# Kernel optimization log

Hardware: AMD Instinct MI355X
Metric: run time of the kernel (lower is better)

Reference implementation:

```python
import jax, jax.numpy as jnp
import numpy as np

B, H, KV, HD, D, S = 8, 32, 8, 128, 4096, 4096
PAST = S - 2  # 4094, cache nearly full
ROPE_THETA = 10000.0


def rotate_half(x):
    h = x.shape[-1] // 2
    return jnp.concatenate([-x[..., h:], x[..., :h]], axis=-1)


def setup_inputs() -> dict:
    key = jax.random.key(0)
    ks = jax.random.split(key, 10)
    hidden_states = jax.random.normal(ks[0], (B, 1, D), jnp.float32)
    # HF additive causal mask for decode: 0 where position is valid, -inf-ish beyond
    pos = jnp.arange(S)
    attention_mask = jnp.broadcast_to(
        jnp.where(pos < PAST + 1, 0.0, -1e9).astype(jnp.float32)[None, None, None, :],
        (B, 1, 1, S),
    )
    # RoPE cos/sin for the single decoded position (position id = PAST)
    inv_freq = 1.0 / (ROPE_THETA ** (jnp.arange(0, HD, 2, dtype=jnp.float32) / HD))
    ang = PAST * inv_freq  # [HD/2]
    emb = jnp.concatenate([ang, ang], axis=-1)  # [HD]
    cos = jnp.broadcast_to(jnp.cos(emb)[None, None, :], (B, 1, HD)).astype(jnp.float32)
    sin = jnp.broadcast_to(jnp.sin(emb)[None, None, :], (B, 1, HD)).astype(jnp.float32)
    past_key = jax.random.normal(ks[1], (B, KV, PAST, HD), jnp.float32)
    past_value = jax.random.normal(ks[2], (B, KV, PAST, HD), jnp.float32)
    k_cache = jax.random.normal(ks[3], (B, KV, S, HD), jnp.float32)
    v_cache = jax.random.normal(ks[4], (B, KV, S, HD), jnp.float32)
    Wq = jax.random.normal(ks[5], (D, H * HD), jnp.float32) * 0.02
    Wk = jax.random.normal(ks[6], (D, KV * HD), jnp.float32) * 0.02
    Wv = jax.random.normal(ks[7], (D, KV * HD), jnp.float32) * 0.02
    Wo = jax.random.normal(ks[8], (H * HD, D), jnp.float32) * 0.02
    return dict(hidden_states=hidden_states, attention_mask=attention_mask, cos=cos,
                sin=sin, past_key=past_key, past_value=past_value,
                k_cache=k_cache, v_cache=v_cache, Wq=Wq, Wk=Wk, Wv=Wv, Wo=Wo)


def reference(hidden_states, attention_mask, cos, sin, past_key, past_value,
              k_cache, v_cache, Wq, Wk, Wv, Wo):
    b = hidden_states.shape[0]
    past_len = past_key.shape[2]  # static
    # q/k/v projections for the single decode token
    q = (hidden_states @ Wq).reshape(b, 1, H, HD).transpose(0, 2, 1, 3)   # [B,H,1,hd]
    k = (hidden_states @ Wk).reshape(b, 1, KV, HD).transpose(0, 2, 1, 3)  # [B,KV,1,hd]
    v = (hidden_states @ Wv).reshape(b, 1, KV, HD).transpose(0, 2, 1, 3)
    # rotary: cos/sin [B,1,hd] -> unsqueeze head dim -> [B,1,1,hd]
    c = cos[:, None, :, :]
    s = sin[:, None, :, :]
    q = q * c + rotate_half(q) * s
    k = k * c + rotate_half(k) * s
    # StaticCache: scatter past K/V into positions [0, past_len), new token at past_len
    kf = k_cache.at[:, :, :past_len, :].set(past_key)
    kf = kf.at[:, :, past_len:past_len + 1, :].set(k)
    vf = v_cache.at[:, :, :past_len, :].set(past_value)
    vf = vf.at[:, :, past_len:past_len + 1, :].set(v)
    # GQA: repeat kv heads
    n_rep = H // KV
    kr = jnp.repeat(kf, n_rep, axis=1)  # [B,H,S,hd]
    vr = jnp.repeat(vf, n_rep, axis=1)
    scores = jnp.einsum('bhqd,bhkd->bhqk', q, kr) / np.float32(np.sqrt(HD))
    scores = scores + attention_mask  # [B,1,1,S] broadcasts over heads
    probs = jax.nn.softmax(scores.astype(jnp.float32), axis=-1).astype(q.dtype)
    out = jnp.einsum('bhqk,bhkd->bhqd', probs, vr)  # [B,H,1,hd]
    out = out.transpose(0, 2, 1, 3).reshape(b, 1, H * HD)
    return out @ Wo  # [B,1,D]
```

## Files before the change

### kernel.cpp

```cpp
#include <hip/hip_runtime.h>

#define BB 8
#define HH 32
#define KVH 8
#define HD 128
#define DD 4096
#define PAST 4094
#define QCOLS 4096
#define KVCOLS 1024
#define NC_QKV 6144
#define DCH 64
#define NDCH 64
#define CHUNK 32
#define NCHUNK 128
#define QSCALE 0.08838834764831845f
#define FIN_PER_B 3584

__global__ __launch_bounds__(256)
void matvec_partial(const float* __restrict__ hin,
                    const float* __restrict__ W0,
                    const float* __restrict__ W1,
                    const float* __restrict__ W2,
                    int c_w1, int c_w2, int NC,
                    float* __restrict__ part)
{
    __shared__ float hl[DCH][BB];
    const int tid = threadIdx.x;
    const int d0 = blockIdx.y * DCH;
    const int cb = blockIdx.x * 512;

    for (int idx = tid; idx < DCH * BB; idx += 256) {
        int dd = idx & (DCH - 1);
        int b = idx >> 6;
        hl[dd][b] = hin[b * DD + d0 + dd];
    }
    __syncthreads();

    const int c = cb + tid * 2;
    const float* W;
    int ldw, cl;
    if (c < c_w1)      { W = W0; ldw = c_w1;        cl = c; }
    else if (c < c_w2) { W = W1; ldw = c_w2 - c_w1; cl = c - c_w1; }
    else               { W = W2; ldw = NC - c_w2;   cl = c - c_w2; }
    const float* wp = W + (size_t)d0 * ldw + cl;

    float2 acc[BB];
    #pragma unroll
    for (int b = 0; b < BB; ++b) { acc[b].x = 0.f; acc[b].y = 0.f; }

    #pragma unroll 8
    for (int dd = 0; dd < DCH; ++dd) {
        float2 w = *(const float2*)wp;
        wp += ldw;
        float hv[8];
        *(float4*)&hv[0] = *(const float4*)&hl[dd][0];
        *(float4*)&hv[4] = *(const float4*)&hl[dd][4];
        #pragma unroll
        for (int b = 0; b < BB; ++b) {
            acc[b].x = fmaf(hv[b], w.x, acc[b].x);
            acc[b].y = fmaf(hv[b], w.y, acc[b].y);
        }
    }

    float* po = part + (size_t)blockIdx.y * (BB * NC) + c;
    #pragma unroll
    for (int b = 0; b < BB; ++b) {
        *(float2*)(po + (size_t)b * NC) = acc[b];
    }
}

__global__ __launch_bounds__(256)
void qkv_finish(const float* __restrict__ part,
                const float* __restrict__ cosv,
                const float* __restrict__ sinv,
                float* __restrict__ qout,
                float* __restrict__ knew,
                float* __restrict__ vnew)
{
    __shared__ float red[4][64][2];
    const int lane = threadIdx.x & 63;
    const int w = threadIdx.x >> 6;
    const int o = blockIdx.x * 64 + lane;
    const int b = o / FIN_PER_B;
    const int r = o - b * FIN_PER_B;

    float s0 = 0.f, s1 = 0.f;
    if (r < 2560) {
        const int hd = r & 63;
        const int head = r >> 6;
        const int c_lo = head * HD + hd;
        const float* p0 = part + (size_t)b * NC_QKV + c_lo;
        const float* p1 = p0 + 64;
        #pragma unroll 16
        for (int i = w * 16; i < w * 16 + 16; ++i) {
            s0 += p0[(size_t)i * (BB * NC_QKV)];
            s1 += p1[(size_t)i * (BB * NC_QKV)];
        }
    } else {
        const int c = r - 2560 + QCOLS + KVCOLS;
        const float* p = part + (size_t)b * NC_QKV + c;
        #pragma unroll 16
        for (int i = w * 16; i < w * 16 + 16; ++i)
            s0 += p[(size_t)i * (BB * NC_QKV)];
    }
    red[w][lane][0] = s0;
    red[w][lane][1] = s1;
    __syncthreads();

    if (threadIdx.x < 64) {
        const float a0 = red[0][lane][0] + red[1][lane][0]
                       + red[2][lane][0] + red[3][lane][0];
        const float a1 = red[0][lane][1] + red[1][lane][1]
                       + red[2][lane][1] + red[3][lane][1];
        if (r < 2560) {
            const int hd = r & 63;
            const int head = r >> 6;
            const int c_lo = head * HD + hd;
            const float cs_lo = cosv[b * HD + hd];
            const float sn_lo = sinv[b * HD + hd];
            const float cs_hi = cosv[b * HD + hd + 64];
            const float sn_hi = sinv[b * HD + hd + 64];
            const float v_lo = fmaf(a0, cs_lo, -a1 * sn_lo);
            const float v_hi = fmaf(a1, cs_hi,  a0 * sn_hi);
            if (c_lo < QCOLS) {
                qout[b * QCOLS + c_lo]      = v_lo * QSCALE;
                qout[b * QCOLS + c_lo + 64] = v_hi * QSCALE;
            } else {
                knew[b * KVCOLS + (c_lo - QCOLS)]      = v_lo;
                knew[b * KVCOLS + (c_lo - QCOLS) + 64] = v_hi;
            }
        } else {
            const int c = r - 2560;
            vnew[b * KVCOLS + c] = a0;
        }
    }
}

__global__ __launch_bounds__(256, 8)
void attn_partial(const float* __restrict__ past_key,
                  const float* __restrict__ past_value,
                  const float* __restrict__ q,
                  const float* __restrict__ knew,
                  const float* __restrict__ vnew,
                  float* __restrict__ pacc,
                  float* __restrict__ pl)
{
    const int pair = blockIdx.x;
    const int wid = threadIdx.x >> 6;
    const int chunk = blockIdx.y * 4 + wid;
    const int b = pair >> 3;
    const int kv = pair & 7;
    const int lane = threadIdx.x & 63;
    const int half = lane >> 5;
    const int lh = lane & 31;

    const float* qb = q + b * QCOLS + (kv * 4) * HD + 4 * lh;
    const float4 qv0 = *(const float4*)(qb);
    const float4 qv1 = *(const float4*)(qb + HD);
    const float4 qv2 = *(const float4*)(qb + 2 * HD);
    const float4 qv3 = *(const float4*)(qb + 3 * HD);

    const float* kb = past_key   + (size_t)pair * PAST * HD;
    const float* vb = past_value + (size_t)pair * PAST * HD;

    float4 acc0 = {0,0,0,0}, acc1 = {0,0,0,0}, acc2 = {0,0,0,0}, acc3 = {0,0,0,0};
    float l0 = 0.f, l1 = 0.f, l2 = 0.f, l3 = 0.f;

    const int jbase = chunk * CHUNK + half;

    if (chunk < NCHUNK - 1) {
        const float* kp = kb + (size_t)jbase * HD + 4 * lh;
        const float* vp = vb + (size_t)jbase * HD + 4 * lh;
        #pragma unroll 4
        for (int it = 0; it < 16; ++it) {
            const float4 kk = *(const float4*)kp;  kp += 2 * HD;
            float s0 = kk.x*qv0.x + kk.y*qv0.y + kk.z*qv0.z + kk.w*qv0.w;
            float s1 = kk.x*qv1.x + kk.y*qv1.y + kk.z*qv1.z + kk.w*qv1.w;
            float s2 = kk.x*qv2.x + kk.y*qv2.y + kk.z*qv2.z + kk.w*qv2.w;
            float s3 = kk.x*qv3.x + kk.y*qv3.y + kk.z*qv3.z + kk.w*qv3.w;
            #pragma unroll
            for (int m = 1; m <= 16; m <<= 1) {
                s0 += __shfl_xor(s0, m, 64);
                s1 += __shfl_xor(s1, m, 64);
                s2 += __shfl_xor(s2, m, 64);
                s3 += __shfl_xor(s3, m, 64);
            }
            const float4 vv = *(const float4*)vp;  vp += 2 * HD;
            const float p0 = __expf(s0);
            const float p1 = __expf(s1);
            const float p2 = __expf(s2);
            const float p3 = __expf(s3);
            l0 += p0; l1 += p1; l2 += p2; l3 += p3;
            acc0.x = fmaf(p0, vv.x, acc0.x); acc0.y = fmaf(p0, vv.y, acc0.y);
            acc0.z = fmaf(p0, vv.z, acc0.z); acc0.w = fmaf(p0, vv.w, acc0.w);
            acc1.x = fmaf(p1, vv.x, acc1.x); acc1.y = fmaf(p1, vv.y, acc1.y);
            acc1.z = fmaf(p1, vv.z, acc1.z); acc1.w = fmaf(p1, vv.w, acc1.w);
            acc2.x = fmaf(p2, vv.x, acc2.x); acc2.y = fmaf(p2, vv.y, acc2.y);
            acc2.z = fmaf(p2, vv.z, acc2.z); acc2.w = fmaf(p2, vv.w, acc2.w);
            acc3.x = fmaf(p3, vv.x, acc3.x); acc3.y = fmaf(p3, vv.y, acc3.y);
            acc3.z = fmaf(p3, vv.z, acc3.z); acc3.w = fmaf(p3, vv.w, acc3.w);
        }
    } else {
        const float* kn = knew + pair * HD;
        const float* vn = vnew + pair * HD;
        #pragma unroll 2
        for (int it = 0; it < 16; ++it) {
            const int j = jbase + it * 2;
            const bool valid = (j <= PAST);
            const float* kp;
            const float* vp;
            if (j < PAST) { kp = kb + (size_t)j * HD; vp = vb + (size_t)j * HD; }
            else          { kp = kn;                   vp = vn; }

            const float4 kk = *(const float4*)(kp + 4 * lh);
            float s0 = kk.x*qv0.x + kk.y*qv0.y + kk.z*qv0.z + kk.w*qv0.w;
            float s1 = kk.x*qv1.x + kk.y*qv1.y + kk.z*qv1.z + kk.w*qv1.w;
            float s2 = kk.x*qv2.x + kk.y*qv2.y + kk.z*qv2.z + kk.w*qv2.w;
            float s3 = kk.x*qv3.x + kk.y*qv3.y + kk.z*qv3.z + kk.w*qv3.w;
            #pragma unroll
            for (int m = 1; m <= 16; m <<= 1) {
                s0 += __shfl_xor(s0, m, 64);
                s1 += __shfl_xor(s1, m, 64);
                s2 += __shfl_xor(s2, m, 64);
                s3 += __shfl_xor(s3, m, 64);
            }
            const float4 vv = *(const float4*)(vp + 4 * lh);
            const float p0 = valid ? __expf(s0) : 0.f;
            const float p1 = valid ? __expf(s1) : 0.f;
            const float p2 = valid ? __expf(s2) : 0.f;
            const float p3 = valid ? __expf(s3) : 0.f;
            l0 += p0; l1 += p1; l2 += p2; l3 += p3;
            acc0.x = fmaf(p0, vv.x, acc0.x); acc0.y = fmaf(p0, vv.y, acc0.y);
            acc0.z = fmaf(p0, vv.z, acc0.z); acc0.w = fmaf(p0, vv.w, acc0.w);
            acc1.x = fmaf(p1, vv.x, acc1.x); acc1.y = fmaf(p1, vv.y, acc1.y);
            acc1.z = fmaf(p1, vv.z, acc1.z); acc1.w = fmaf(p1, vv.w, acc1.w);
            acc2.x = fmaf(p2, vv.x, acc2.x); acc2.y = fmaf(p2, vv.y, acc2.y);
            acc2.z = fmaf(p2, vv.z, acc2.z); acc2.w = fmaf(p2, vv.w, acc2.w);
            acc3.x = fmaf(p3, vv.x, acc3.x); acc3.y = fmaf(p3, vv.y, acc3.y);
            acc3.z = fmaf(p3, vv.z, acc3.z); acc3.w = fmaf(p3, vv.w, acc3.w);
        }
    }

    l0 += __shfl_xor(l0, 32, 64);
    l1 += __shfl_xor(l1, 32, 64);
    l2 += __shfl_xor(l2, 32, 64);
    l3 += __shfl_xor(l3, 32, 64);
    acc0.x += __shfl_xor(acc0.x, 32, 64); acc0.y += __shfl_xor(acc0.y, 32, 64);
    acc0.z += __shfl_xor(acc0.z, 32, 64); acc0.w += __shfl_xor(acc0.w, 32, 64);
    acc1.x += __shfl_xor(acc1.x, 32, 64); acc1.y += __shfl_xor(acc1.y, 32, 64);
    acc1.z += __shfl_xor(acc1.z, 32, 64); acc1.w += __shfl_xor(acc1.w, 32, 64);
    acc2.x += __shfl_xor(acc2.x, 32, 64); acc2.y += __shfl_xor(acc2.y, 32, 64);
    acc2.z += __shfl_xor(acc2.z, 32, 64); acc2.w += __shfl_xor(acc2.w, 32, 64);
    acc3.x += __shfl_xor(acc3.x, 32, 64); acc3.y += __shfl_xor(acc3.y, 32, 64);
    acc3.z += __shfl_xor(acc3.z, 32, 64); acc3.w += __shfl_xor(acc3.w, 32, 64);

    if (half == 0) {
        float* po = pacc + (((size_t)pair * NCHUNK + chunk) * 4) * HD + 4 * lh;
        *(float4*)(po)          = acc0;
        *(float4*)(po + HD)     = acc1;
        *(float4*)(po + 2*HD)   = acc2;
        *(float4*)(po + 3*HD)   = acc3;
        if (lh == 0) {
            float* plo = pl + ((size_t)pair * NCHUNK + chunk) * 4;
            plo[0] = l0; plo[1] = l1; plo[2] = l2; plo[3] = l3;
        }
    }
}

__global__ __launch_bounds__(256)
void attn_combine(const float* __restrict__ pacc,
                  const float* __restrict__ pl,
                  float* __restrict__ attn_out)
{
    __shared__ float racc[4][64];
    __shared__ float rl[4];
    const int lane = threadIdx.x & 63;
    const int w = threadIdx.x >> 6;
    const int o = blockIdx.x * 64 + lane;
    const int d = o & 127;
    const int h = (o >> 7) & 31;
    const int b = o >> 12;
    const int kv = h >> 2;
    const int qi = h & 3;
    const int pair = b * 8 + kv;

    const float* pa  = pacc + ((size_t)pair * NCHUNK * 4 + qi) * HD + d;
    const float* pls = pl + (size_t)pair * NCHUNK * 4 + qi;
    float acc = 0.f, lsum = 0.f;
    #pragma unroll 8
    for (int c = w * 32; c < w * 32 + 32; ++c) {
        acc  += pa[(size_t)c * 4 * HD];
        lsum += pls[c * 4];
    }
    racc[w][lane] = acc;
    if (lane == 0) rl[w] = lsum;
    __syncthreads();
    if (threadIdx.x < 64) {
        const float a = racc[0][lane] + racc[1][lane]
                      + racc[2][lane] + racc[3][lane];
        const float L = rl[0] + rl[1] + rl[2] + rl[3];
        attn_out[b * QCOLS + h * HD + d] = a / L;
    }
}

__global__ __launch_bounds__(256)
void wo_finish(const float* __restrict__ part, float* __restrict__ out)
{
    __shared__ float red[4][64];
    const int lane = threadIdx.x & 63;
    const int w = threadIdx.x >> 6;
    const int o = blockIdx.x * 64 + lane;
    const float* p = part + o;
    float s = 0.f;
    #pragma unroll 16
    for (int i = w * 16; i < w * 16 + 16; ++i)
        s += p[(size_t)i * (BB * QCOLS)];
    red[w][lane] = s;
    __syncthreads();
    if (threadIdx.x < 64) {
        out[o] = red[0][lane] + red[1][lane] + red[2][lane] + red[3][lane];
    }
}

extern "C" void kernel_launch(void* const* d_in, const int* in_sizes, int n_in,
                              void* d_out, int out_size, void* d_ws, size_t ws_size,
                              hipStream_t stream)
{
    (void)in_sizes; (void)n_in; (void)out_size; (void)ws_size;
    const float* hidden     = (const float*)d_in[0];
    const float* cosv       = (const float*)d_in[2];
    const float* sinv       = (const float*)d_in[3];
    const float* past_key   = (const float*)d_in[4];
    const float* past_value = (const float*)d_in[5];
    const float* Wq = (const float*)d_in[8];
    const float* Wk = (const float*)d_in[9];
    const float* Wv = (const float*)d_in[10];
    const float* Wo = (const float*)d_in[11];
    float* out = (float*)d_out;
    float* ws  = (float*)d_ws;

    float* qkv_part = ws;
    float* qrope    = qkv_part + (size_t)NDCH * BB * NC_QKV;
    float* knew     = qrope + BB * QCOLS;
    float* vnew     = knew + BB * KVCOLS;
    float* pacc     = vnew + BB * KVCOLS;
    float* pl       = pacc + (size_t)64 * NCHUNK * 4 * HD;
    float* attn_out = pl + (size_t)64 * NCHUNK * 4;
    float* wo_part  = qkv_part;

    matvec_partial<<<dim3(12, NDCH), 256, 0, stream>>>(
        hidden, Wq, Wk, Wv, 4096, 5120, NC_QKV, qkv_part);
    qkv_finish<<<(BB * FIN_PER_B) / 64, 256, 0, stream>>>(
        qkv_part, cosv, sinv, qrope, knew, vnew);
    attn_partial<<<dim3(64, NCHUNK / 4), 256, 0, stream>>>(
        past_key, past_value, qrope, knew, vnew, pacc, pl);
    attn_combine<<<(BB * HH * HD) / 64, 256, 0, stream>>>(pacc, pl, attn_out);
    matvec_partial<<<dim3(8, NDCH), 256, 0, stream>>>(
        attn_out, Wo, Wo, Wo, 4096, 5120, QCOLS, wo_part);
    wo_finish<<<(BB * QCOLS) / 64, 256, 0, stream>>>(wo_part, out);
}
```

Before: 122.2 us.

## Reduce attention partials in-block via shared memory and hoist V loads

The attention partial kernel now uses 512-thread blocks, each covering 8 chunks. The 8 wave results are summed in shared memory before writing, so the global partial buffer shrinks from 128 to 16 entries per pair and the combine kernel reads far less. The V loads are also issued alongside the K loads, ahead of the shuffle reduction, to overlap their latency. The cost is a block-wide barrier, extra shared memory, and half the threads sitting idle during the in-block reduction.

Measured after the change: 146.2 us. 19.6% more time.

```diff
diff --git a/kernel.cpp b/kernel.cpp
--- a/kernel.cpp
+++ b/kernel.cpp
@@ -12,6 +12,7 @@
 #define DCH 64
 #define NDCH 64
 #define CHUNK 32
+#define YBLK 16
 #define NCHUNK 128
 #define QSCALE 0.08838834764831845f
 #define FIN_PER_B 3584
@@ -136,7 +137,7 @@
     }
 }
 
-__global__ __launch_bounds__(256, 8)
+__global__ __launch_bounds__(512, 8)
 void attn_partial(const float* __restrict__ past_key,
                   const float* __restrict__ past_value,
                   const float* __restrict__ q,
@@ -147,7 +148,7 @@
 {
     const int pair = blockIdx.x;
     const int wid = threadIdx.x >> 6;
-    const int chunk = blockIdx.y * 4 + wid;
+    const int chunk = blockIdx.y * 8 + wid;
     const int b = pair >> 3;
     const int kv = pair & 7;
     const int lane = threadIdx.x & 63;
@@ -174,6 +175,7 @@
         #pragma unroll 4
         for (int it = 0; it < 16; ++it) {
             const float4 kk = *(const float4*)kp;  kp += 2 * HD;
+            const float4 vv = *(const float4*)vp;  vp += 2 * HD;
             float s0 = kk.x*qv0.x + kk.y*qv0.y + kk.z*qv0.z + kk.w*qv0.w;
             float s1 = kk.x*qv1.x + kk.y*qv1.y + kk.z*qv1.z + kk.w*qv1.w;
             float s2 = kk.x*qv2.x + kk.y*qv2.y + kk.z*qv2.z + kk.w*qv2.w;
@@ -185,7 +187,6 @@
                 s2 += __shfl_xor(s2, m, 64);
                 s3 += __shfl_xor(s3, m, 64);
             }
-            const float4 vv = *(const float4*)vp;  vp += 2 * HD;
             const float p0 = __expf(s0);
             const float p1 = __expf(s1);
             const float p2 = __expf(s2);
@@ -213,6 +214,7 @@
             else          { kp = kn;                   vp = vn; }
 
             const float4 kk = *(const float4*)(kp + 4 * lh);
+            const float4 vv = *(const float4*)(vp + 4 * lh);
             float s0 = kk.x*qv0.x + kk.y*qv0.y + kk.z*qv0.z + kk.w*qv0.w;
             float s1 = kk.x*qv1.x + kk.y*qv1.y + kk.z*qv1.z + kk.w*qv1.w;
             float s2 = kk.x*qv2.x + kk.y*qv2.y + kk.z*qv2.z + kk.w*qv2.w;
@@ -224,7 +226,6 @@
                 s2 += __shfl_xor(s2, m, 64);
                 s3 += __shfl_xor(s3, m, 64);
             }
-            const float4 vv = *(const float4*)(vp + 4 * lh);
             const float p0 = valid ? __expf(s0) : 0.f;
             const float p1 = valid ? __expf(s1) : 0.f;
             const float p2 = valid ? __expf(s2) : 0.f;
@@ -254,15 +255,35 @@
     acc3.x += __shfl_xor(acc3.x, 32, 64); acc3.y += __shfl_xor(acc3.y, 32, 64);
     acc3.z += __shfl_xor(acc3.z, 32, 64); acc3.w += __shfl_xor(acc3.w, 32, 64);
 
+    __shared__ float lacc[8][4][HD];
+    __shared__ float ll[8][4];
     if (half == 0) {
-        float* po = pacc + (((size_t)pair * NCHUNK + chunk) * 4) * HD + 4 * lh;
-        *(float4*)(po)          = acc0;
-        *(float4*)(po + HD)     = acc1;
-        *(float4*)(po + 2*HD)   = acc2;
-        *(float4*)(po + 3*HD)   = acc3;
+        *(float4*)&lacc[wid][0][4 * lh] = acc0;
+        *(float4*)&lacc[wid][1][4 * lh] = acc1;
+        *(float4*)&lacc[wid][2][4 * lh] = acc2;
+        *(float4*)&lacc[wid][3][4 * lh] = acc3;
         if (lh == 0) {
-            float* plo = pl + ((size_t)pair * NCHUNK + chunk) * 4;
-            plo[0] = l0; plo[1] = l1; plo[2] = l2; plo[3] = l3;
+            ll[wid][0] = l0; ll[wid][1] = l1; ll[wid][2] = l2; ll[wid][3] = l3;
+        }
+    }
+    __syncthreads();
+    if (threadIdx.x < 256) {
+        const int head = threadIdx.x >> 6;
+        const int d2 = lane * 2;
+        float ax = 0.f, ay = 0.f;
+        #pragma unroll
+        for (int w = 0; w < 8; ++w) {
+            ax += lacc[w][head][d2];
+            ay += lacc[w][head][d2 + 1];
+        }
+        float* po = pacc + (((size_t)pair * YBLK + blockIdx.y) * 4 + head) * HD + d2;
+        float2 r; r.x = ax; r.y = ay;
+        *(float2*)po = r;
+        if (lane == 0) {
+            float L = 0.f;
+            #pragma unroll
+            for (int w = 0; w < 8; ++w) L += ll[w][head];
+            pl[((size_t)pair * YBLK + blockIdx.y) * 4 + head] = L;
         }
     }
 }
@@ -284,11 +305,11 @@
     const int qi = h & 3;
     const int pair = b * 8 + kv;
 
-    const float* pa  = pacc + ((size_t)pair * NCHUNK * 4 + qi) * HD + d;
-    const float* pls = pl + (size_t)pair * NCHUNK * 4 + qi;
+    const float* pa  = pacc + ((size_t)pair * YBLK * 4 + qi) * HD + d;
+    const float* pls = pl + (size_t)pair * YBLK * 4 + qi;
     float acc = 0.f, lsum = 0.f;
-    #pragma unroll 8
-    for (int c = w * 32; c < w * 32 + 32; ++c) {
+    #pragma unroll
+    for (int c = w * 4; c < w * 4 + 4; ++c) {
         acc  += pa[(size_t)c * 4 * HD];
         lsum += pls[c * 4];
     }
@@ -344,15 +365,15 @@
     float* knew     = qrope + BB * QCOLS;
     float* vnew     = knew + BB * KVCOLS;
     float* pacc     = vnew + BB * KVCOLS;
-    float* pl       = pacc + (size_t)64 * NCHUNK * 4 * HD;
-    float* attn_out = pl + (size_t)64 * NCHUNK * 4;
+    float* pl       = pacc + (size_t)64 * YBLK * 4 * HD;
+    float* attn_out = pl + (size_t)64 * YBLK * 4;
     float* wo_part  = qkv_part;
 
     matvec_partial<<<dim3(12, NDCH), 256, 0, stream>>>(
         hidden, Wq, Wk, Wv, 4096, 5120, NC_QKV, qkv_part);
     qkv_finish<<<(BB * FIN_PER_B) / 64, 256, 0, stream>>>(
         qkv_part, cosv, sinv, qrope, knew, vnew);
-    attn_partial<<<dim3(64, NCHUNK / 4), 256, 0, stream>>>(
+    attn_partial<<<dim3(64, YBLK), 512, 0, stream>>>(
         past_key, past_value, qrope, knew, vnew, pacc, pl);
     attn_combine<<<(BB * HH * HD) / 64, 256, 0, stream>>>(pacc, pl, attn_out);
     matvec_partial<<<dim3(8, NDCH), 256, 0, stream>>>(
```
